# Optimization experiments

Measured on AMD Instinct MI355X. Metric: run time of the kernel, lower is better.

## Reference

```python
import jax, jax.numpy as jnp
import numpy as np

E, D, F = 32, 2048, 768  # num_experts, hidden_size, intermediate_size
B, S, TOPK = 2, 1024, 8
T = B * S


def setup_inputs() -> dict:
    key = jax.random.key(0)
    k1, k2, k3, k4, k5 = jax.random.split(key, 5)
    hidden_states = jax.random.normal(k1, (B, S, D), dtype=jnp.float32)
    routing_weights = jax.random.uniform(k2, (T, E), dtype=jnp.float32)
    router_indices = jax.random.randint(k3, (T, TOPK), 0, E)
    gate_up_proj = jax.random.normal(k4, (E, D, 2 * F), dtype=jnp.float32) * 0.02
    down_proj = jax.random.normal(k5, (E, F, D), dtype=jnp.float32) * 0.02
    return {
        "hidden_states": hidden_states,
        "routing_weights": routing_weights,
        "router_indices": router_indices,
        "gate_up_proj": gate_up_proj,
        "down_proj": down_proj,
    }


def reference(hidden_states, routing_weights, router_indices, gate_up_proj, down_proj):
    batch_size = hidden_states.shape[0]
    x = hidden_states.reshape(-1, D)  # (T, D)
    gate_up = jnp.einsum('TD,EDF->TEF', x, gate_up_proj)  # (T, E, 2F)
    gate, up = jnp.split(gate_up, 2, axis=-1)
    gated = up * jax.nn.silu(gate)  # (T, E, F)
    next_states = jnp.einsum('TEF,EFD->TED', gated, down_proj)  # (T, E, D)
    next_states = (next_states * routing_weights[..., None]).sum(axis=1)  # (T, D)
    return next_states.reshape(batch_size, -1, D)
```

## Files before the change

kernel.cpp:

```cpp
#include <hip/hip_runtime.h>
#include <stdint.h>

#define NE 32
#define ND 2048
#define NF 768
#define NF2 1536
#define NT 2048
#define NEF (NE * NF)
#define KH 12288

#define BM 128
#define BN 64
#define BK 32
#define BSTR 40

typedef __attribute__((ext_vector_type(8))) short short8;
typedef __attribute__((ext_vector_type(4))) float floatx4;

__device__ __forceinline__ unsigned pk_bf16(float a, float b) {
  union { float f; unsigned u; } ua, ub;
  ua.f = a; ub.f = b;
  unsigned ra = (ua.u + 0x7fffu + ((ua.u >> 16) & 1u)) >> 16;
  unsigned rb = (ub.u + 0x7fffu + ((ub.u >> 16) & 1u)) & 0xffff0000u;
  return ra | rb;
}
__device__ __forceinline__ unsigned short bf16_1(float a) {
  union { float f; unsigned u; } ua; ua.f = a;
  return (unsigned short)((ua.u + 0x7fffu + ((ua.u >> 16) & 1u)) >> 16);
}

#define GLOAD_LDS16(g, l)                                                     \
  __builtin_amdgcn_global_load_lds(                                           \
      (const __attribute__((address_space(1))) void*)(g),                     \
      (__attribute__((address_space(3))) void*)(l), 16, 0, 0)

__global__ void k_cvt_x(const float* __restrict__ x, unsigned short* __restrict__ xb, int n4) {
  int i = blockIdx.x * blockDim.x + threadIdx.x;
  if (i < n4) {
    float4 v = ((const float4*)x)[i];
    uint2 o;
    o.x = pk_bf16(v.x, v.y);
    o.y = pk_bf16(v.z, v.w);
    ((uint2*)xb)[i] = o;
  }
}

__global__ void k_trans(const float* __restrict__ in, unsigned short* __restrict__ out,
                        int R, int C, size_t zstride) {
  __shared__ float sT[64][65];
  in  += (size_t)blockIdx.z * zstride;
  out += (size_t)blockIdx.z * zstride;
  const int r0 = blockIdx.y * 64, c0 = blockIdx.x * 64;
  const int t = threadIdx.x;
  const int lrow = t >> 4, lc4 = (t & 15) * 4;
#pragma unroll
  for (int i = 0; i < 4; i++) {
    float4 v = *(const float4*)&in[(size_t)(r0 + lrow + i * 16) * C + c0 + lc4];
    sT[lrow + i * 16][lc4 + 0] = v.x;
    sT[lrow + i * 16][lc4 + 1] = v.y;
    sT[lrow + i * 16][lc4 + 2] = v.z;
    sT[lrow + i * 16][lc4 + 3] = v.w;
  }
  __syncthreads();
  const int c = t >> 2, rg = (t & 3) * 16;
  uint4 o0, o1;
  o0.x = pk_bf16(sT[rg + 0][c],  sT[rg + 1][c]);
  o0.y = pk_bf16(sT[rg + 2][c],  sT[rg + 3][c]);
  o0.z = pk_bf16(sT[rg + 4][c],  sT[rg + 5][c]);
  o0.w = pk_bf16(sT[rg + 6][c],  sT[rg + 7][c]);
  o1.x = pk_bf16(sT[rg + 8][c],  sT[rg + 9][c]);
  o1.y = pk_bf16(sT[rg + 10][c], sT[rg + 11][c]);
  o1.z = pk_bf16(sT[rg + 12][c], sT[rg + 13][c]);
  o1.w = pk_bf16(sT[rg + 14][c], sT[rg + 15][c]);
  unsigned short* op = &out[(size_t)(c0 + c) * R + r0 + rg];
  ((uint4*)op)[0] = o0;
  ((uint4*)op)[1] = o1;
}

__global__ __launch_bounds__(256, 2) void k_gemm1b(
    const unsigned short* __restrict__ xb,
    const unsigned short* __restrict__ w1t,
    const float* __restrict__ rw,
    unsigned short* __restrict__ gws,
    int e0)
{
  __shared__ unsigned short sA[BM * BK];
  __shared__ unsigned short sG[BN * BK];
  __shared__ unsigned short sU[BN * BK];
  __shared__ float srw[BM];

  const int el  = blockIdx.y;
  const int e   = e0 + el;
  const int mt  = blockIdx.x & 15;
  const int nt  = blockIdx.x >> 4;
  const int m0  = mt * BM, n0 = nt * BN;
  const int tid = threadIdx.x;
  const int wid = tid >> 6, lane = tid & 63;
  const int wm = wid >> 1, wn = wid & 1;
  const int l15 = lane & 15, q = lane >> 4;

  if (tid < BM) srw[tid] = rw[(size_t)(m0 + tid) * NE + e];

  floatx4 accG[4][2], accU[4][2];
#pragma unroll
  for (int i = 0; i < 4; i++)
#pragma unroll
    for (int j = 0; j < 2; j++) {
      accG[i][j] = (floatx4){0.f, 0.f, 0.f, 0.f};
      accU[i][j] = (floatx4){0.f, 0.f, 0.f, 0.f};
    }

  const unsigned short* w1e = w1t + (size_t)el * NF2 * ND;

  const int koff = (lane & 3) * 8;
  const unsigned short* aptr = xb + (size_t)(m0 + wid * 32 + (lane >> 2)) * ND + koff;
  unsigned short* aLds = &sA[wid * 32 * BK];
  const unsigned short* gptr = w1e + (size_t)(n0 + wid * 16 + (lane >> 2)) * ND + koff;
  const unsigned short* uptr = gptr + (size_t)NF * ND;
  unsigned short* gLds = &sG[wid * 16 * BK];
  unsigned short* uLds = &sU[wid * 16 * BK];

  for (int kb = 0; kb < ND / BK; ++kb) {
    __syncthreads();
    GLOAD_LDS16(aptr + kb * BK, aLds);
    GLOAD_LDS16(aptr + kb * BK + 16 * ND, aLds + 16 * BK);
    GLOAD_LDS16(gptr + kb * BK, gLds);
    GLOAD_LDS16(uptr + kb * BK, uLds);
    __syncthreads();

    short8 bg0 = *(const short8*)&sG[(wn * 32 + 0  + l15) * BK + q * 8];
    short8 bg1 = *(const short8*)&sG[(wn * 32 + 16 + l15) * BK + q * 8];
    short8 bu0 = *(const short8*)&sU[(wn * 32 + 0  + l15) * BK + q * 8];
    short8 bu1 = *(const short8*)&sU[(wn * 32 + 16 + l15) * BK + q * 8];
#pragma unroll
    for (int i = 0; i < 4; i++) {
      short8 af = *(const short8*)&sA[(wm * 64 + i * 16 + l15) * BK + q * 8];
      accG[i][0] = __builtin_amdgcn_mfma_f32_16x16x32_bf16(af, bg0, accG[i][0], 0, 0, 0);
      accG[i][1] = __builtin_amdgcn_mfma_f32_16x16x32_bf16(af, bg1, accG[i][1], 0, 0, 0);
      accU[i][0] = __builtin_amdgcn_mfma_f32_16x16x32_bf16(af, bu0, accU[i][0], 0, 0, 0);
      accU[i][1] = __builtin_amdgcn_mfma_f32_16x16x32_bf16(af, bu1, accU[i][1], 0, 0, 0);
    }
  }

  const size_t obase = (size_t)m0 * NEF + (size_t)e * NF + n0 + wn * 32;
#pragma unroll
  for (int i = 0; i < 4; i++)
#pragma unroll
    for (int j = 0; j < 2; j++)
#pragma unroll
      for (int r = 0; r < 4; r++) {
        int row = wm * 64 + i * 16 + q * 4 + r;
        float g = accG[i][j][r];
        float u = accU[i][j][r];
        float sig = __builtin_amdgcn_rcpf(1.f + __expf(-g));
        float val = u * g * sig * srw[row];
        gws[obase + (size_t)row * NEF + j * 16 + l15] = bf16_1(val);
      }
}

__global__ __launch_bounds__(256, 2) void k_gemm2b(
    const unsigned short* __restrict__ gb,
    const unsigned short* __restrict__ w2t,
    float* __restrict__ out,
    int kbase)
{
  __shared__ unsigned short sA[BM * BK];
  __shared__ unsigned short sB[BN * BK];

  const int mt = blockIdx.x & 15;
  const int nt = blockIdx.x >> 4;
  const int m0 = mt * BM, n0 = nt * BN;
  const int tid = threadIdx.x;
  const int wid = tid >> 6, lane = tid & 63;
  const int wm = wid >> 1, wn = wid & 1;
  const int l15 = lane & 15, q = lane >> 4;

  const int kb0 = blockIdx.y * (KH / BK / 2);
  const int kb1 = kb0 + (KH / BK / 2);

  floatx4 acc[4][2];
#pragma unroll
  for (int i = 0; i < 4; i++)
#pragma unroll
    for (int j = 0; j < 2; j++) acc[i][j] = (floatx4){0.f, 0.f, 0.f, 0.f};

  const int koff = (lane & 3) * 8;
  const unsigned short* aptr = gb + (size_t)(m0 + wid * 32 + (lane >> 2)) * NEF + kbase + koff;
  unsigned short* aLds = &sA[wid * 32 * BK];
  const unsigned short* bptr = w2t + (size_t)(n0 + wid * 16 + (lane >> 2)) * KH + koff;
  unsigned short* bLds = &sB[wid * 16 * BK];

  for (int kb = kb0; kb < kb1; ++kb) {
    __syncthreads();
    GLOAD_LDS16(aptr + kb * BK, aLds);
    GLOAD_LDS16(aptr + kb * BK + 16 * NEF, aLds + 16 * BK);
    GLOAD_LDS16(bptr + kb * BK, bLds);
    __syncthreads();

    short8 b0 = *(const short8*)&sB[(wn * 32 + 0  + l15) * BK + q * 8];
    short8 b1 = *(const short8*)&sB[(wn * 32 + 16 + l15) * BK + q * 8];
#pragma unroll
    for (int i = 0; i < 4; i++) {
      short8 af = *(const short8*)&sA[(wm * 64 + i * 16 + l15) * BK + q * 8];
      acc[i][0] = __builtin_amdgcn_mfma_f32_16x16x32_bf16(af, b0, acc[i][0], 0, 0, 0);
      acc[i][1] = __builtin_amdgcn_mfma_f32_16x16x32_bf16(af, b1, acc[i][1], 0, 0, 0);
    }
  }

#pragma unroll
  for (int i = 0; i < 4; i++)
#pragma unroll
    for (int j = 0; j < 2; j++)
#pragma unroll
      for (int r = 0; r < 4; r++) {
        int row = wm * 64 + i * 16 + q * 4 + r;
        unsafeAtomicAdd(&out[(size_t)(m0 + row) * ND + n0 + wn * 32 + j * 16 + l15],
                        acc[i][j][r]);
      }
}

__global__ __launch_bounds__(256, 2) void k_gemm1_legacy(
    const unsigned short* __restrict__ xb, const float* __restrict__ w1,
    const float* __restrict__ rw, unsigned short* __restrict__ gws)
{
  __shared__ unsigned short sA[BM * BK];
  __shared__ unsigned short sG[BN * BSTR];
  __shared__ unsigned short sU[BN * BSTR];
  __shared__ float srw[BM];
  const int e = blockIdx.y, mt = blockIdx.x & 15, nt = blockIdx.x >> 4;
  const int m0 = mt * BM, n0 = nt * BN;
  const int tid = threadIdx.x, wid = tid >> 6, lane = tid & 63;
  const int wm = wid >> 1, wn = wid & 1, l15 = lane & 15, q = lane >> 4;
  if (tid < BM) srw[tid] = rw[(size_t)(m0 + tid) * NE + e];
  const float* w1e = w1 + (size_t)e * ND * (2 * NF);
  floatx4 accG[4][2], accU[4][2];
#pragma unroll
  for (int i = 0; i < 4; i++)
#pragma unroll
    for (int j = 0; j < 2; j++) {
      accG[i][j] = (floatx4){0.f, 0.f, 0.f, 0.f};
      accU[i][j] = (floatx4){0.f, 0.f, 0.f, 0.f};
    }
  const int arow = wid * 32 + (lane >> 2), akoff = (lane & 3) * 8;
  const unsigned short* aptr = xb + (size_t)(m0 + arow) * ND + akoff;
  unsigned short* aLds = &sA[wid * 32 * BK];
  const float* gptr0 = w1e + (size_t)(wid * 8) * (2 * NF) + n0 + lane;
  for (int kb = 0; kb < ND / BK; ++kb) {
    const float* gp = gptr0 + (size_t)kb * BK * (2 * NF);
    float gv[8], uv[8];
#pragma unroll
    for (int r = 0; r < 8; r++) {
      gv[r] = gp[(size_t)r * (2 * NF)];
      uv[r] = gp[(size_t)r * (2 * NF) + NF];
    }
    __syncthreads();
    GLOAD_LDS16(aptr + kb * BK, aLds);
    GLOAD_LDS16(aptr + kb * BK + 16 * ND, aLds + 16 * BK);
    uint4 wg, wu;
    wg.x = pk_bf16(gv[0], gv[1]); wg.y = pk_bf16(gv[2], gv[3]);
    wg.z = pk_bf16(gv[4], gv[5]); wg.w = pk_bf16(gv[6], gv[7]);
    wu.x = pk_bf16(uv[0], uv[1]); wu.y = pk_bf16(uv[2], uv[3]);
    wu.z = pk_bf16(uv[4], uv[5]); wu.w = pk_bf16(uv[6], uv[7]);
    *((uint4*)&sG[lane * BSTR + wid * 8]) = wg;
    *((uint4*)&sU[lane * BSTR + wid * 8]) = wu;
    __syncthreads();
    short8 bg0 = *(const short8*)&sG[(wn * 32 + 0  + l15) * BSTR + q * 8];
    short8 bg1 = *(const short8*)&sG[(wn * 32 + 16 + l15) * BSTR + q * 8];
    short8 bu0 = *(const short8*)&sU[(wn * 32 + 0  + l15) * BSTR + q * 8];
    short8 bu1 = *(const short8*)&sU[(wn * 32 + 16 + l15) * BSTR + q * 8];
#pragma unroll
    for (int i = 0; i < 4; i++) {
      short8 af = *(const short8*)&sA[(wm * 64 + i * 16 + l15) * BK + q * 8];
      accG[i][0] = __builtin_amdgcn_mfma_f32_16x16x32_bf16(af, bg0, accG[i][0], 0, 0, 0);
      accG[i][1] = __builtin_amdgcn_mfma_f32_16x16x32_bf16(af, bg1, accG[i][1], 0, 0, 0);
      accU[i][0] = __builtin_amdgcn_mfma_f32_16x16x32_bf16(af, bu0, accU[i][0], 0, 0, 0);
      accU[i][1] = __builtin_amdgcn_mfma_f32_16x16x32_bf16(af, bu1, accU[i][1], 0, 0, 0);
    }
  }
  const size_t obase = (size_t)m0 * NEF + (size_t)e * NF + n0 + wn * 32;
#pragma unroll
  for (int i = 0; i < 4; i++)
#pragma unroll
    for (int j = 0; j < 2; j++)
#pragma unroll
      for (int r = 0; r < 4; r++) {
        int row = wm * 64 + i * 16 + q * 4 + r;
        float g = accG[i][j][r], u = accU[i][j][r];
        float sig = __builtin_amdgcn_rcpf(1.f + __expf(-g));
        gws[obase + (size_t)row * NEF + j * 16 + l15] = bf16_1(u * g * sig * srw[row]);
      }
}

__global__ __launch_bounds__(256, 2) void k_gemm2_legacy(
    const unsigned short* __restrict__ gb, const float* __restrict__ w2,
    float* __restrict__ out)
{
  __shared__ unsigned short sA[BM * BK];
  __shared__ unsigned short sB[BN * BSTR];
  const int mt = blockIdx.x & 15, nt = blockIdx.x >> 4;
  const int m0 = mt * BM, n0 = nt * BN;
  const int tid = threadIdx.x, wid = tid >> 6, lane = tid & 63;
  const int wm = wid >> 1, wn = wid & 1, l15 = lane & 15, q = lane >> 4;
  const int kb0 = blockIdx.y * (NEF / BK / 4), kb1 = kb0 + (NEF / BK / 4);
  floatx4 acc[4][2];
#pragma unroll
  for (int i = 0; i < 4; i++)
#pragma unroll
    for (int j = 0; j < 2; j++) acc[i][j] = (floatx4){0.f, 0.f, 0.f, 0.f};
  const int arow = wid * 32 + (lane >> 2), akoff = (lane & 3) * 8;
  const unsigned short* aptr = gb + (size_t)(m0 + arow) * NEF + akoff;
  unsigned short* aLds = &sA[wid * 32 * BK];
  const float* bptr0 = w2 + (size_t)(wid * 8) * ND + n0 + lane;
  for (int kb = kb0; kb < kb1; ++kb) {
    const float* bp = bptr0 + (size_t)kb * BK * ND;
    float bv[8];
#pragma unroll
    for (int r = 0; r < 8; r++) bv[r] = bp[(size_t)r * ND];
    __syncthreads();
    GLOAD_LDS16(aptr + kb * BK, aLds);
    GLOAD_LDS16(aptr + kb * BK + 16 * NEF, aLds + 16 * BK);
    uint4 wb;
    wb.x = pk_bf16(bv[0], bv[1]); wb.y = pk_bf16(bv[2], bv[3]);
    wb.z = pk_bf16(bv[4], bv[5]); wb.w = pk_bf16(bv[6], bv[7]);
    *((uint4*)&sB[lane * BSTR + wid * 8]) = wb;
    __syncthreads();
    short8 b0 = *(const short8*)&sB[(wn * 32 + 0  + l15) * BSTR + q * 8];
    short8 b1 = *(const short8*)&sB[(wn * 32 + 16 + l15) * BSTR + q * 8];
#pragma unroll
    for (int i = 0; i < 4; i++) {
      short8 af = *(const short8*)&sA[(wm * 64 + i * 16 + l15) * BK + q * 8];
      acc[i][0] = __builtin_amdgcn_mfma_f32_16x16x32_bf16(af, b0, acc[i][0], 0, 0, 0);
      acc[i][1] = __builtin_amdgcn_mfma_f32_16x16x32_bf16(af, b1, acc[i][1], 0, 0, 0);
    }
  }
#pragma unroll
  for (int i = 0; i < 4; i++)
#pragma unroll
    for (int j = 0; j < 2; j++)
#pragma unroll
      for (int r = 0; r < 4; r++) {
        int row = wm * 64 + i * 16 + q * 4 + r;
        unsafeAtomicAdd(&out[(size_t)(m0 + row) * ND + n0 + wn * 32 + j * 16 + l15],
                        acc[i][j][r]);
      }
}

extern "C" void kernel_launch(void* const* d_in, const int* in_sizes, int n_in,
                              void* d_out, int out_size, void* d_ws, size_t ws_size,
                              hipStream_t stream) {
  const float* x  = (const float*)d_in[0];
  const float* rw = (const float*)d_in[1];
  const float* w1 = (const float*)d_in[3];
  const float* w2 = (const float*)d_in[4];
  float* out = (float*)d_out;

  unsigned short* xb  = (unsigned short*)d_ws;
  unsigned short* gb  = xb + (size_t)NT * ND;
  unsigned short* wtb = gb + (size_t)NT * NEF;
  const size_t WS_NEED = ((size_t)NT * ND + (size_t)NT * NEF +
                          (size_t)8 * NF2 * ND) * 2;

  hipMemsetAsync(out, 0, (size_t)out_size * sizeof(float), stream);
  k_cvt_x<<<(NT * ND / 4 + 255) / 256, 256, 0, stream>>>(x, xb, NT * ND / 4);

  if (ws_size >= WS_NEED) {
    for (int qc = 0; qc < 4; ++qc) {
      dim3 gt(NF2 / 64, ND / 64, 8);
      k_trans<<<gt, 256, 0, stream>>>(w1 + (size_t)qc * 8 * ND * NF2, wtb,
                                      ND, NF2, (size_t)ND * NF2);
      dim3 g1(16 * (NF / BN), 8);
      k_gemm1b<<<g1, 256, 0, stream>>>(xb, wtb, rw, gb, qc * 8);
    }
    for (int h = 0; h < 2; ++h) {
      dim3 gt(ND / 64, KH / 64, 1);
      k_trans<<<gt, 256, 0, stream>>>(w2 + (size_t)h * KH * ND, wtb, KH, ND, 0);
      dim3 g2(16 * (ND / BN), 2);
      k_gemm2b<<<g2, 256, 0, stream>>>(gb, wtb, out, h * KH);
    }
  } else {
    dim3 gA(16 * (NF / BN), NE);
    k_gemm1_legacy<<<gA, 256, 0, stream>>>(xb, w1, rw, gb);
    dim3 gB(16 * (ND / BN), 4);
    k_gemm2_legacy<<<gB, 256, 0, stream>>>(gb, w2, out);
  }
}
```

Before: 1.546 ms.

## Transpose all weights up front and run single full-size GEMM launches

When the workspace is large enough, all expert weights for both projections are transposed to bf16 in one launch each, and each GEMM then runs as a single launch over all experts instead of four plus two chunked launches. The goal is to cut launch count and the serialization between transpose and GEMM chunks, and to expose more blocks per launch. Launch bounds are also raised to target three blocks per CU, which may push register usage down and risk spills. The cost is a much larger workspace requirement; the chunked path stays as a fallback.

```diff
diff --git a/kernel.cpp b/kernel.cpp
--- a/kernel.cpp
+++ b/kernel.cpp
@@ -77,7 +77,7 @@
   ((uint4*)op)[1] = o1;
 }
 
-__global__ __launch_bounds__(256, 2) void k_gemm1b(
+__global__ __launch_bounds__(256, 3) void k_gemm1b(
     const unsigned short* __restrict__ xb,
     const unsigned short* __restrict__ w1t,
     const float* __restrict__ rw,
@@ -158,7 +158,8 @@
       }
 }
 
-__global__ __launch_bounds__(256, 2) void k_gemm2b(
+template<int KSTRIDE, int HITERS>
+__global__ __launch_bounds__(256, 3) void k_gemm2b(
     const unsigned short* __restrict__ gb,
     const unsigned short* __restrict__ w2t,
     float* __restrict__ out,
@@ -175,8 +176,8 @@
   const int wm = wid >> 1, wn = wid & 1;
   const int l15 = lane & 15, q = lane >> 4;
 
-  const int kb0 = blockIdx.y * (KH / BK / 2);
-  const int kb1 = kb0 + (KH / BK / 2);
+  const int kb0 = blockIdx.y * HITERS;
+  const int kb1 = kb0 + HITERS;
 
   floatx4 acc[4][2];
 #pragma unroll
@@ -187,7 +188,7 @@
   const int koff = (lane & 3) * 8;
   const unsigned short* aptr = gb + (size_t)(m0 + wid * 32 + (lane >> 2)) * NEF + kbase + koff;
   unsigned short* aLds = &sA[wid * 32 * BK];
-  const unsigned short* bptr = w2t + (size_t)(n0 + wid * 16 + (lane >> 2)) * KH + koff;
+  const unsigned short* bptr = w2t + (size_t)(n0 + wid * 16 + (lane >> 2)) * KSTRIDE + koff;
   unsigned short* bLds = &sB[wid * 16 * BK];
 
   for (int kb = kb0; kb < kb1; ++kb) {
@@ -357,13 +358,34 @@
   unsigned short* xb  = (unsigned short*)d_ws;
   unsigned short* gb  = xb + (size_t)NT * ND;
   unsigned short* wtb = gb + (size_t)NT * NEF;
+  unsigned short* w1t = wtb;
+  unsigned short* w2t = w1t + (size_t)NE * NF2 * ND;
+  const size_t WS_FULL = ((size_t)NT * ND + (size_t)NT * NEF +
+                          (size_t)NE * NF2 * ND + (size_t)ND * NEF) * 2;
   const size_t WS_NEED = ((size_t)NT * ND + (size_t)NT * NEF +
                           (size_t)8 * NF2 * ND) * 2;
 
   hipMemsetAsync(out, 0, (size_t)out_size * sizeof(float), stream);
   k_cvt_x<<<(NT * ND / 4 + 255) / 256, 256, 0, stream>>>(x, xb, NT * ND / 4);
 
-  if (ws_size >= WS_NEED) {
+  if (ws_size >= WS_FULL) {
+    {
+      dim3 gt(NF2 / 64, ND / 64, NE);
+      k_trans<<<gt, 256, 0, stream>>>(w1, w1t, ND, NF2, (size_t)ND * NF2);
+    }
+    {
+      dim3 gt(ND / 64, NEF / 64, 1);
+      k_trans<<<gt, 256, 0, stream>>>(w2, w2t, NEF, ND, 0);
+    }
+    {
+      dim3 g1(16 * (NF / BN), NE);
+      k_gemm1b<<<g1, 256, 0, stream>>>(xb, w1t, rw, gb, 0);
+    }
+    {
+      dim3 g2(16 * (ND / BN), 2);
+      k_gemm2b<NEF, NEF / BK / 2><<<g2, 256, 0, stream>>>(gb, w2t, out, 0);
+    }
+  } else if (ws_size >= WS_NEED) {
     for (int qc = 0; qc < 4; ++qc) {
       dim3 gt(NF2 / 64, ND / 64, 8);
       k_trans<<<gt, 256, 0, stream>>>(w1 + (size_t)qc * 8 * ND * NF2, wtb,
@@ -375,7 +397,7 @@
       dim3 gt(ND / 64, KH / 64, 1);
       k_trans<<<gt, 256, 0, stream>>>(w2 + (size_t)h * KH * ND, wtb, KH, ND, 0);
       dim3 g2(16 * (ND / BN), 2);
-      k_gemm2b<<<g2, 256, 0, stream>>>(gb, wtb, out, h * KH);
+      k_gemm2b<KH, KH / BK / 2><<<g2, 256, 0, stream>>>(gb, wtb, out, h * KH);
     }
   } else {
     dim3 gA(16 * (NF / BN), NE);
```

Measured after the change: 1.503 ms. -2.8%, faster.
